# Performance work log

Measured on AMD Instinct MI355X. Metric: run time of the kernel, lower is better.

## Reference

```python
import jax, jax.numpy as jnp
import numpy as np

IN, H, OUT = 88, 200, 88


def lstm_layer(x, w_ih, w_hh, b_ih, b_hh):
    # x: [T, B, in]; weights in torch layout: w_ih [4H, in], w_hh [4H, H]
    # gate order (torch): i, f, g, o
    gx = jnp.einsum('tbi,gi->tbg', x, w_ih) + (b_ih + b_hh)  # precompute input gates
    B = x.shape[1]
    h0 = jnp.zeros((B, w_hh.shape[1]), x.dtype)
    c0 = jnp.zeros((B, w_hh.shape[1]), x.dtype)

    def step(carry, gxt):
        h, c = carry
        gates = gxt + h @ w_hh.T
        i, f, g, o = jnp.split(gates, 4, axis=-1)
        i = jax.nn.sigmoid(i)
        f = jax.nn.sigmoid(f)
        g = jnp.tanh(g)
        o = jax.nn.sigmoid(o)
        c = f * c + i * g
        h = o * jnp.tanh(c)
        return (h, c), h

    (hT, cT), ys = jax.lax.scan(step, (h0, c0), gx)
    return ys, hT, cT


def setup_inputs() -> dict:
    key = jax.random.key(0)
    ks = jax.random.split(key, 11)
    s = 1.0 / np.sqrt(H)
    u = lambda k, shape: jax.random.uniform(k, shape, jnp.float32, -s, s)
    T, B = 2048, 128
    x = (jax.random.uniform(ks[0], (T, B, IN)) > 0.9).astype(jnp.float32)  # sparse piano roll
    return {
        'x': x,
        'w_ih0': u(ks[1], (4 * H, IN)), 'w_hh0': u(ks[2], (4 * H, H)),
        'b_ih0': u(ks[3], (4 * H,)), 'b_hh0': u(ks[4], (4 * H,)),
        'w_ih1': u(ks[5], (4 * H, H)), 'w_hh1': u(ks[6], (4 * H, H)),
        'b_ih1': u(ks[7], (4 * H,)), 'b_hh1': u(ks[8], (4 * H,)),
        'w_fc': u(ks[9], (OUT, H)), 'b_fc': u(ks[10], (OUT,)),
    }


def reference(x, w_ih0, w_hh0, b_ih0, b_hh0, w_ih1, w_hh1, b_ih1, b_hh1, w_fc, b_fc):
    y0, h0n, c0n = lstm_layer(x, w_ih0, w_hh0, b_ih0, b_hh0)
    y1, h1n, c1n = lstm_layer(y0, w_ih1, w_hh1, b_ih1, b_hh1)
    out = jax.nn.sigmoid(jnp.einsum('tbh,oh->tbo', y1, w_fc) + b_fc)
    hn = jnp.stack([h0n, h1n])  # [2, B, H]
    cn = jnp.stack([c0n, c1n])
    return out, hn, cn
```

## Files before the change

### kernel.cpp

```cpp
#include <hip/hip_runtime.h>
#include <cstdint>
#include <cstddef>


#define TS    2048
#define BB    128
#define IN_D  88
#define HID   200
#define OUT_D 88
#define KX    96
#define KH    224
#define RING  4
#define FR    16
#define FSTR  32

typedef __attribute__((ext_vector_type(8))) short short8;
typedef __attribute__((ext_vector_type(4))) float f32x4;

constexpr int NW0 = 13, NW1 = 13;
constexpr int NWORK = NW0 + NW1 + 1;

__device__ inline unsigned short f2bf(float f){
  union{float f; unsigned u;} v; v.f = f;
  unsigned r = v.u + 0x7FFFu + ((v.u >> 16) & 1u);
  return (unsigned short)(r >> 16);
}
__device__ inline float sigf(float x){ return 1.0f/(1.0f + __expf(-x)); }
__device__ inline float tanhf2(float x){ return 2.0f/(1.0f + __expf(-2.0f*x)) - 1.0f; }

__device__ inline unsigned ld_flag(const unsigned* p){
  return __hip_atomic_load(p, __ATOMIC_RELAXED, __HIP_MEMORY_SCOPE_AGENT);
}
__device__ inline void post1(unsigned* p){
  __hip_atomic_fetch_add(p, 1u, __ATOMIC_RELAXED, __HIP_MEMORY_SCOPE_AGENT);
}
__device__ inline unsigned* fsl(unsigned* base, int t){ return base + (size_t)(t & (FR-1))*FSTR; }
__device__ inline unsigned ftg(int t, int nw){ return (unsigned)((t/FR + 1)*nw); }

__device__ inline void wg_wait2(int tid, unsigned* p0, unsigned v0,
                                unsigned* p1, unsigned v1){
  if (tid < 64 && (p0 || p1)){
    int n = 0;
    for(;;){
      unsigned a0 = p0 ? ld_flag(p0) : 0xFFFFFFFFu;
      unsigned a1 = p1 ? ld_flag(p1) : 0xFFFFFFFFu;
      bool ok = true;
      if (p0 && a0 < v0) ok = false;
      if (p1 && a1 < v1) ok = false;
      if (ok || ++n > 4000) break;
      __builtin_amdgcn_s_sleep(1);
    }
  }
  __syncthreads();
}

__device__ inline short8 loadB(const unsigned short* buf, int b, int kt, int q){
  const unsigned long long* p =
      (const unsigned long long*)(buf + ((size_t)kt*BB + b)*32 + q*8);
  unsigned long long lo = __hip_atomic_load(p,   __ATOMIC_RELAXED, __HIP_MEMORY_SCOPE_AGENT);
  unsigned long long hi = __hip_atomic_load(p+1, __ATOMIC_RELAXED, __HIP_MEMORY_SCOPE_AGENT);
  union{ unsigned long long u[2]; short8 s; } v; v.u[0]=lo; v.u[1]=hi;
  return v.s;
}

__device__ inline void cvt_x(const float4* pa, const float4* pb, int q, short8* xf){
  #pragma unroll
  for (int kt = 0; kt < 3; ++kt){
    int k = kt*32 + q*8;
    short8 r = {0,0,0,0,0,0,0,0};
    if (k + 8 <= IN_D){
      r[0]=(short)f2bf(pa[kt].x); r[1]=(short)f2bf(pa[kt].y);
      r[2]=(short)f2bf(pa[kt].z); r[3]=(short)f2bf(pa[kt].w);
      r[4]=(short)f2bf(pb[kt].x); r[5]=(short)f2bf(pb[kt].y);
      r[6]=(short)f2bf(pb[kt].z); r[7]=(short)f2bf(pb[kt].w);
    }
    xf[kt] = r;
  }
}

template<int ROLE>
__device__ void run_role(int j0,
    const float* __restrict__ xin,
    const float* __restrict__ wi, const float* __restrict__ wh,
    const float* __restrict__ bi, const float* __restrict__ bh,
    float* __restrict__ out,
    unsigned short* h0buf, unsigned short* h1buf,
    unsigned* f0p, unsigned* f0c, unsigned* f1p, unsigned* f1c,
    unsigned* f1g, unsigned* fFg,
    short* w_s, float* bias_s, unsigned short* hT)
{
  constexpr int ROWS = (ROLE==2)?96:64;
  constexpr int MT   = (ROLE==2)?6:4;
  constexpr int KTOT = (ROLE==0)?10:(ROLE==1?14:7);
  const int tid = threadIdx.x;

  constexpr int TOTW = KTOT*4*MT*16*8;
  for (int idx = tid; idx < TOTW; idx += 512){
    int e    = idx & 7;
    int nn_s = (idx >> 3) & 15;
    int rest = idx >> 7;
    int mt   = rest % MT;
    int qk   = rest / MT;
    int q_s  = qk & 3;
    int ktf  = qk >> 2;
    int r = mt*16 + nn_s;
    int k = ktf*32 + q_s*8 + e;
    float v = 0.f;
    if (ROLE == 2){
      if (r < OUT_D && k < HID) v = wi[r*HID + k];
    } else {
      int j = j0 + (r >> 2), g = r & 3;
      if (j < HID){
        int gr = g*HID + j;
        if (ROLE == 0){
          if (k < IN_D)                   v = wi[gr*IN_D + k];
          else if (k >= KX && k < KX+HID) v = wh[gr*HID + (k-KX)];
        } else {
          if (k < HID)                    v = wi[gr*HID + k];
          else if (k >= KH && k < KH+HID) v = wh[gr*HID + (k-KH)];
        }
      }
    }
    w_s[idx] = (short)f2bf(v);
  }
  for (int r = tid; r < ROWS; r += 512){
    float bv = 0.f;
    if (ROLE == 2){ if (r < OUT_D) bv = bi[r]; }
    else { int j = j0 + (r>>2), g = r&3; if (j < HID){ int gr = g*HID+j; bv = bi[gr] + bh[gr]; } }
    bias_s[r] = bv;
  }
  __syncthreads();

  const int lane = tid & 63;
  const int wv   = tid >> 6;
  const int q    = lane >> 4;
  const int nn   = lane & 15;
  const int b    = wv*16 + nn;

  const int wbase = (q*MT*16 + nn)*8;
  #define WS_FRAG(ktf, mt) (*(const short8*)&w_s[wbase + ((ktf)*4*MT + (mt))*128])

  float c[MT], hl[MT];
  #pragma unroll
  for (int i=0;i<MT;i++){ c[i]=0.f; hl[i]=0.f; }

  short8 xf[3];
  float4 pa[3], pb[3];
  if (ROLE == 0){
    #pragma unroll
    for (int kt=0;kt<3;kt++){
      int k = kt*32 + q*8;
      if (k + 8 <= IN_D){
        const float* xp = xin + (size_t)b*IN_D + k;
        pa[kt] = *(const float4*)xp; pb[kt] = *(const float4*)(xp + 4);
      }
    }
    cvt_x(pa, pb, q, xf);
  }

  for (int t = 0; t < TS; ++t){
    f32x4 acc[MT];
    #pragma unroll
    for (int mt=0; mt<MT; ++mt){
      #pragma unroll
      for (int r=0;r<4;r++) acc[mt][r] = bias_s[mt*16 + q*4 + r];
    }

    if (ROLE == 0){
      #pragma unroll
      for (int kt=0; kt<3; ++kt){
        #pragma unroll
        for (int mt=0; mt<MT; ++mt){
          acc[mt] = __builtin_amdgcn_mfma_f32_16x16x32_bf16(WS_FRAG(kt,mt), xf[kt], acc[mt], 0, 0, 0);
        }
      }
      if (t + 1 < TS){
        #pragma unroll
        for (int kt=0;kt<3;kt++){
          int k = kt*32 + q*8;
          if (k + 8 <= IN_D){
            const float* xp = xin + ((size_t)(t+1)*BB + b)*IN_D + k;
            pa[kt] = *(const float4*)xp; pb[kt] = *(const float4*)(xp + 4);
          }
        }
      }
      unsigned *p0=nullptr,*p1=nullptr; unsigned v0=0,v1=0;
      if (t >= 1){   p0 = fsl(f0p, t-1);    v0 = ftg(t-1, NW0); }
      if (t >= RING){p1 = fsl(f1g, t-RING); v1 = ftg(t-RING, NW1); }
      wg_wait2(tid, p0, v0, p1, v1);
      const unsigned short* hs = h0buf + (size_t)((t-1)&(RING-1))*(BB*KH);
      short8 bfr[7];
      #pragma unroll
      for (int kt=0;kt<7;kt++) bfr[kt] = loadB(hs, b, kt, q);
      #pragma unroll
      for (int kt=0;kt<7;kt++){
        #pragma unroll
        for (int mt=0; mt<MT; ++mt){
          acc[mt] = __builtin_amdgcn_mfma_f32_16x16x32_bf16(WS_FRAG(3+kt,mt), bfr[kt], acc[mt], 0, 0, 0);
        }
      }
    } else if (ROLE == 1){
      {
        unsigned *p1=nullptr; unsigned v1=0;
        if (t >= RING){ p1 = fsl(fFg, t-RING); v1 = ftg(t-RING, 1); }
        wg_wait2(tid, fsl(f0c, t), ftg(t, NW0), p1, v1);
      }
      const unsigned short* hs0 = h0buf + (size_t)(t&(RING-1))*(BB*KH);
      short8 bfr0[7];
      #pragma unroll
      for (int kt=0;kt<7;kt++) bfr0[kt] = loadB(hs0, b, kt, q);
      {
        unsigned *p0=nullptr; unsigned v0=0;
        if (t >= 1){ p0 = fsl(f1p, t-1); v0 = ftg(t-1, NW1); }
        wg_wait2(tid, p0, v0, nullptr, 0);
      }
      const unsigned short* hs1 = h1buf + (size_t)((t-1)&(RING-1))*(BB*KH);
      short8 bfr1[7];
      #pragma unroll
      for (int kt=0;kt<7;kt++) bfr1[kt] = loadB(hs1, b, kt, q);
      #pragma unroll
      for (int kt=0;kt<7;kt++){
        #pragma unroll
        for (int mt=0; mt<MT; ++mt){
          acc[mt] = __builtin_amdgcn_mfma_f32_16x16x32_bf16(WS_FRAG(kt,mt), bfr0[kt], acc[mt], 0, 0, 0);
        }
      }
      __syncthreads();
      if (tid == 0) post1(fsl(f1g, t));
      #pragma unroll
      for (int kt=0;kt<7;kt++){
        #pragma unroll
        for (int mt=0; mt<MT; ++mt){
          acc[mt] = __builtin_amdgcn_mfma_f32_16x16x32_bf16(WS_FRAG(7+kt,mt), bfr1[kt], acc[mt], 0, 0, 0);
        }
      }
    } else {
      wg_wait2(tid, fsl(f1c, t), ftg(t, NW1), nullptr, 0);
      const unsigned short* hs1 = h1buf + (size_t)(t&(RING-1))*(BB*KH);
      short8 bfr[7];
      #pragma unroll
      for (int kt=0;kt<7;kt++) bfr[kt] = loadB(hs1, b, kt, q);
      #pragma unroll
      for (int kt=0;kt<7;kt++){
        #pragma unroll
        for (int mt=0; mt<MT; ++mt){
          acc[mt] = __builtin_amdgcn_mfma_f32_16x16x32_bf16(WS_FRAG(kt,mt), bfr[kt], acc[mt], 0, 0, 0);
        }
      }
      __syncthreads();
      if (tid == 0) post1(fsl(fFg, t));
      #pragma unroll
      for (int mt=0; mt<MT; ++mt){
        #pragma unroll
        for (int r=0;r<4;r++){
          int o = mt*16 + q*4 + r;
          if (o < OUT_D) out[((size_t)t*BB + b)*OUT_D + o] = sigf(acc[mt][r]);
        }
      }
      continue;
    }

    #pragma unroll
    for (int mt=0; mt<MT; ++mt){
      float ii = sigf(acc[mt][0]);
      float ff = sigf(acc[mt][1]);
      float gg = tanhf2(acc[mt][2]);
      float oo = sigf(acc[mt][3]);
      c[mt] = ff*c[mt] + ii*gg;
      float h = oo * tanhf2(c[mt]);
      hl[mt] = h;
      hT[b*16 + mt*4 + q] = f2bf(h);
    }
    __syncthreads();
    {
      int bb = tid >> 2, ch = tid & 3;
      if (j0 + ch*4 < HID){
        unsigned long long v = *(const unsigned long long*)&hT[bb*16 + ch*4];
        int kt = j0 >> 5, off = j0 & 31;
        unsigned short* dst = (ROLE==0 ? h0buf : h1buf)
                            + (size_t)(t&(RING-1))*(BB*KH)
                            + ((size_t)kt*BB + bb)*32 + off + ch*4;
        __hip_atomic_store((unsigned long long*)dst, v,
                           __ATOMIC_RELAXED, __HIP_MEMORY_SCOPE_AGENT);
      }
    }
    asm volatile("s_waitcnt vmcnt(0)" ::: "memory");
    __syncthreads();
    if (tid == 0){
      if (ROLE == 0){ post1(fsl(f0p, t)); post1(fsl(f0c, t)); }
      else          { post1(fsl(f1p, t)); post1(fsl(f1c, t)); }
    }
    if (ROLE == 0) cvt_x(pa, pb, q, xf);
  }

  if (ROLE < 2){
    size_t base = (size_t)TS*BB*OUT_D;
    float* hn = out + base + (size_t)ROLE*(BB*HID);
    float* cn = out + base + 2*(size_t)BB*HID + (size_t)ROLE*(BB*HID);
    #pragma unroll
    for (int mt=0; mt<MT; ++mt){
      int unit = j0 + mt*4 + q;
      if (unit < HID){
        hn[b*HID + unit] = hl[mt];
        cn[b*HID + unit] = c[mt];
      }
    }
  }
  #undef WS_FRAG
}

__global__ __launch_bounds__(512, 2) void lstm_net(
    const float* __restrict__ x,
    const float* __restrict__ wih0, const float* __restrict__ whh0,
    const float* __restrict__ bih0, const float* __restrict__ bhh0,
    const float* __restrict__ wih1, const float* __restrict__ whh1,
    const float* __restrict__ bih1, const float* __restrict__ bhh1,
    const float* __restrict__ wfc,  const float* __restrict__ bfc,
    float* __restrict__ out,
    unsigned short* h0buf, unsigned short* h1buf,
    unsigned* f0p, unsigned* f0c, unsigned* f1p, unsigned* f1c,
    unsigned* f1g, unsigned* fFg)
{
  __shared__ short w_s[64*456];
  __shared__ float bias_s[96];
  __shared__ unsigned short hT[128*16];
  int wg = blockIdx.x;
  if (wg < NW0){
    run_role<0>(wg*16, x, wih0, whh0, bih0, bhh0, out, h0buf, h1buf,
                f0p, f0c, f1p, f1c, f1g, fFg, w_s, bias_s, hT);
  } else if (wg < NW0+NW1){
    run_role<1>((wg-NW0)*16, x, wih1, whh1, bih1, bhh1, out, h0buf, h1buf,
                f0p, f0c, f1p, f1c, f1g, fFg, w_s, bias_s, hT);
  } else {
    run_role<2>(0, x, wfc, nullptr, bfc, nullptr, out, h0buf, h1buf,
                f0p, f0c, f1p, f1c, f1g, fFg, w_s, bias_s, hT);
  }
}

extern "C" void kernel_launch(void* const* d_in, const int* in_sizes, int n_in,
                              void* d_out, int out_size, void* d_ws, size_t ws_size,
                              hipStream_t stream) {
  const float* x    = (const float*)d_in[0];
  const float* wih0 = (const float*)d_in[1];
  const float* whh0 = (const float*)d_in[2];
  const float* bih0 = (const float*)d_in[3];
  const float* bhh0 = (const float*)d_in[4];
  const float* wih1 = (const float*)d_in[5];
  const float* whh1 = (const float*)d_in[6];
  const float* bih1 = (const float*)d_in[7];
  const float* bhh1 = (const float*)d_in[8];
  const float* wfc  = (const float*)d_in[9];
  const float* bfc  = (const float*)d_in[10];
  float* out = (float*)d_out;

  char* ws = (char*)d_ws;
  const size_t HSZ = (size_t)RING * BB * KH * 2;
  const size_t FSZ = (size_t)FR * FSTR * 4;
  unsigned short* h0 = (unsigned short*)(ws + 0);
  unsigned short* h1 = (unsigned short*)(ws + HSZ);
  unsigned* f0p = (unsigned*)(ws + 2*HSZ + 0*FSZ);
  unsigned* f0c = (unsigned*)(ws + 2*HSZ + 1*FSZ);
  unsigned* f1p = (unsigned*)(ws + 2*HSZ + 2*FSZ);
  unsigned* f1c = (unsigned*)(ws + 2*HSZ + 3*FSZ);
  unsigned* f1g = (unsigned*)(ws + 2*HSZ + 4*FSZ);
  unsigned* fFg = (unsigned*)(ws + 2*HSZ + 5*FSZ);

  hipMemsetAsync(d_ws, 0, 2*HSZ + 6*FSZ, stream);
  hipLaunchKernelGGL(lstm_net, dim3(NWORK), dim3(512), 0, stream,
      x, wih0, whh0, bih0, bhh0, wih1, whh1, bih1, bhh1, wfc, bfc,
      out, h0, h1, f0p, f0c, f1p, f1c, f1g, fFg);
}
```

Measured before the change: 12.33 ms.

## Split layer-1 input projection into dedicated producer workgroups feeding recurrent workgroups

Adds 13 new workgroups that compute the layer-1 input-gate projection (W_ih1·h0 + bias) per timestep and write fp32 partial gates into a ring buffer with per-slice flags. The layer-1 recurrent workgroups now load only W_hh1 (halving their K depth), read the precomputed gates, and run just the h1 recurrent MFMAs. This takes the input projection off the layer-1 critical path so layer 1 no longer serialises on both matmuls each step. In exchange it adds extra global traffic, more flags and workgroups, and a longer spin timeout.

```diff
diff --git a/kernel.cpp b/kernel.cpp
--- a/kernel.cpp
+++ b/kernel.cpp
@@ -17,8 +17,8 @@
 typedef __attribute__((ext_vector_type(8))) short short8;
 typedef __attribute__((ext_vector_type(4))) float f32x4;
 
-constexpr int NW0 = 13, NW1 = 13;
-constexpr int NWORK = NW0 + NW1 + 1;
+constexpr int NW0 = 13, NWP = 13, NW1 = 13;
+constexpr int NWORK = NW0 + NWP + NW1 + 1;
 
 __device__ inline unsigned short f2bf(float f){
   union{float f; unsigned u;} v; v.f = f;
@@ -31,11 +31,21 @@
 __device__ inline unsigned ld_flag(const unsigned* p){
   return __hip_atomic_load(p, __ATOMIC_RELAXED, __HIP_MEMORY_SCOPE_AGENT);
 }
+__device__ inline void st_flag(unsigned* p, unsigned v){
+  __hip_atomic_store(p, v, __ATOMIC_RELAXED, __HIP_MEMORY_SCOPE_AGENT);
+}
 __device__ inline void post1(unsigned* p){
   __hip_atomic_fetch_add(p, 1u, __ATOMIC_RELAXED, __HIP_MEMORY_SCOPE_AGENT);
 }
 __device__ inline unsigned* fsl(unsigned* base, int t){ return base + (size_t)(t & (FR-1))*FSTR; }
 __device__ inline unsigned ftg(int t, int nw){ return (unsigned)((t/FR + 1)*nw); }
+
+__device__ inline unsigned long long ld64(const unsigned long long* p){
+  return __hip_atomic_load(p, __ATOMIC_RELAXED, __HIP_MEMORY_SCOPE_AGENT);
+}
+__device__ inline void st64(unsigned long long* p, unsigned long long v){
+  __hip_atomic_store(p, v, __ATOMIC_RELAXED, __HIP_MEMORY_SCOPE_AGENT);
+}
 
 __device__ inline void wg_wait2(int tid, unsigned* p0, unsigned v0,
                                 unsigned* p1, unsigned v1){
@@ -47,7 +57,7 @@
       bool ok = true;
       if (p0 && a0 < v0) ok = false;
       if (p1 && a1 < v1) ok = false;
-      if (ok || ++n > 4000) break;
+      if (ok || ++n > 20000) break;
       __builtin_amdgcn_s_sleep(1);
     }
   }
@@ -57,8 +67,8 @@
 __device__ inline short8 loadB(const unsigned short* buf, int b, int kt, int q){
   const unsigned long long* p =
       (const unsigned long long*)(buf + ((size_t)kt*BB + b)*32 + q*8);
-  unsigned long long lo = __hip_atomic_load(p,   __ATOMIC_RELAXED, __HIP_MEMORY_SCOPE_AGENT);
-  unsigned long long hi = __hip_atomic_load(p+1, __ATOMIC_RELAXED, __HIP_MEMORY_SCOPE_AGENT);
+  unsigned long long lo = ld64(p);
+  unsigned long long hi = ld64(p+1);
   union{ unsigned long long u[2]; short8 s; } v; v.u[0]=lo; v.u[1]=hi;
   return v.s;
 }
@@ -79,19 +89,19 @@
 }
 
 template<int ROLE>
-__device__ void run_role(int j0,
+__device__ void run_role(int j0, int pj,
     const float* __restrict__ xin,
     const float* __restrict__ wi, const float* __restrict__ wh,
     const float* __restrict__ bi, const float* __restrict__ bh,
     float* __restrict__ out,
-    unsigned short* h0buf, unsigned short* h1buf,
+    unsigned short* h0buf, unsigned short* h1buf, float* gxbuf,
     unsigned* f0p, unsigned* f0c, unsigned* f1p, unsigned* f1c,
-    unsigned* f1g, unsigned* fFg,
+    unsigned* f1g, unsigned* fFg, unsigned* fGp, unsigned* fGg,
     short* w_s, float* bias_s, unsigned short* hT)
 {
   constexpr int ROWS = (ROLE==2)?96:64;
   constexpr int MT   = (ROLE==2)?6:4;
-  constexpr int KTOT = (ROLE==0)?10:(ROLE==1?14:7);
+  constexpr int KTOT = (ROLE==0)?10:7;
   const int tid = threadIdx.x;
 
   constexpr int TOTW = KTOT*4*MT*16*8;
@@ -108,17 +118,18 @@
     float v = 0.f;
     if (ROLE == 2){
       if (r < OUT_D && k < HID) v = wi[r*HID + k];
-    } else {
+    } else if (ROLE == 0){
       int j = j0 + (r >> 2), g = r & 3;
       if (j < HID){
         int gr = g*HID + j;
-        if (ROLE == 0){
-          if (k < IN_D)                   v = wi[gr*IN_D + k];
-          else if (k >= KX && k < KX+HID) v = wh[gr*HID + (k-KX)];
-        } else {
-          if (k < HID)                    v = wi[gr*HID + k];
-          else if (k >= KH && k < KH+HID) v = wh[gr*HID + (k-KH)];
-        }
+        if (k < IN_D)                   v = wi[gr*IN_D + k];
+        else if (k >= KX && k < KX+HID) v = wh[gr*HID + (k-KX)];
+      }
+    } else {
+      int j = j0 + (r >> 2), g = r & 3;
+      if (j < HID && k < HID){
+        int gr = g*HID + j;
+        v = wi[gr*HID + k];
       }
     }
     w_s[idx] = (short)f2bf(v);
@@ -126,7 +137,10 @@
   for (int r = tid; r < ROWS; r += 512){
     float bv = 0.f;
     if (ROLE == 2){ if (r < OUT_D) bv = bi[r]; }
-    else { int j = j0 + (r>>2), g = r&3; if (j < HID){ int gr = g*HID+j; bv = bi[gr] + bh[gr]; } }
+    else if (ROLE != 1){
+      int j = j0 + (r>>2), g = r&3;
+      if (j < HID){ int gr = g*HID+j; bv = bi[gr] + bh[gr]; }
+    }
     bias_s[r] = bv;
   }
   __syncthreads();
@@ -159,11 +173,48 @@
   }
 
   for (int t = 0; t < TS; ++t){
+    if (ROLE == 3){
+      f32x4 acc[4];
+      #pragma unroll
+      for (int mt=0; mt<4; ++mt){
+        #pragma unroll
+        for (int r=0;r<4;r++) acc[mt][r] = bias_s[mt*16 + q*4 + r];
+      }
+      {
+        unsigned *p1=nullptr; unsigned v1=0;
+        if (t >= RING){ p1 = fsl(fGg, t-RING)+pj; v1 = (unsigned)(t-RING+1); }
+        wg_wait2(tid, fsl(f0c, t), ftg(t, NW0), p1, v1);
+      }
+      const unsigned short* hs0 = h0buf + (size_t)(t&(RING-1))*(BB*KH);
+      short8 bfr0[7];
+      #pragma unroll
+      for (int kt=0;kt<7;kt++) bfr0[kt] = loadB(hs0, b, kt, q);
+      #pragma unroll
+      for (int kt=0;kt<7;kt++){
+        #pragma unroll
+        for (int mt=0; mt<4; ++mt){
+          acc[mt] = __builtin_amdgcn_mfma_f32_16x16x32_bf16(WS_FRAG(kt,mt), bfr0[kt], acc[mt], 0, 0, 0);
+        }
+      }
+      float* gd = gxbuf + (((size_t)(t&(RING-1))*NWP + pj)*512 + tid)*16;
+      union{ f32x4 v[4]; unsigned long long u[8]; } g;
+      #pragma unroll
+      for (int mt=0;mt<4;mt++) g.v[mt]=acc[mt];
+      #pragma unroll
+      for (int i=0;i<8;i++) st64(((unsigned long long*)gd)+i, g.u[i]);
+      asm volatile("s_waitcnt vmcnt(0)" ::: "memory");
+      __syncthreads();
+      if (tid == 0){ st_flag(fsl(fGp,t)+pj, (unsigned)(t+1)); post1(fsl(f1g,t)); }
+      continue;
+    }
+
     f32x4 acc[MT];
-    #pragma unroll
-    for (int mt=0; mt<MT; ++mt){
-      #pragma unroll
-      for (int r=0;r<4;r++) acc[mt][r] = bias_s[mt*16 + q*4 + r];
+    if (ROLE != 1){
+      #pragma unroll
+      for (int mt=0; mt<MT; ++mt){
+        #pragma unroll
+        for (int r=0;r<4;r++) acc[mt][r] = bias_s[mt*16 + q*4 + r];
+      }
     }
 
     if (ROLE == 0){
@@ -186,7 +237,7 @@
       }
       unsigned *p0=nullptr,*p1=nullptr; unsigned v0=0,v1=0;
       if (t >= 1){   p0 = fsl(f0p, t-1);    v0 = ftg(t-1, NW0); }
-      if (t >= RING){p1 = fsl(f1g, t-RING); v1 = ftg(t-RING, NW1); }
+      if (t >= RING){p1 = fsl(f1g, t-RING); v1 = ftg(t-RING, NWP); }
       wg_wait2(tid, p0, v0, p1, v1);
       const unsigned short* hs = h0buf + (size_t)((t-1)&(RING-1))*(BB*KH);
       short8 bfr[7];
@@ -203,35 +254,24 @@
       {
         unsigned *p1=nullptr; unsigned v1=0;
         if (t >= RING){ p1 = fsl(fFg, t-RING); v1 = ftg(t-RING, 1); }
-        wg_wait2(tid, fsl(f0c, t), ftg(t, NW0), p1, v1);
-      }
-      const unsigned short* hs0 = h0buf + (size_t)(t&(RING-1))*(BB*KH);
-      short8 bfr0[7];
-      #pragma unroll
-      for (int kt=0;kt<7;kt++) bfr0[kt] = loadB(hs0, b, kt, q);
-      {
-        unsigned *p0=nullptr; unsigned v0=0;
-        if (t >= 1){ p0 = fsl(f1p, t-1); v0 = ftg(t-1, NW1); }
-        wg_wait2(tid, p0, v0, nullptr, 0);
-      }
+        wg_wait2(tid, fsl(fGp,t)+pj, (unsigned)(t+1), p1, v1);
+      }
+      if (t >= 1) wg_wait2(tid, fsl(f1p, t-1), ftg(t-1, NW1), nullptr, 0);
+      const float* gs = gxbuf + (((size_t)(t&(RING-1))*NWP + pj)*512 + tid)*16;
+      union{ f32x4 v[4]; unsigned long long u[8]; } g;
+      #pragma unroll
+      for (int i=0;i<8;i++) g.u[i] = ld64(((const unsigned long long*)gs)+i);
       const unsigned short* hs1 = h1buf + (size_t)((t-1)&(RING-1))*(BB*KH);
       short8 bfr1[7];
       #pragma unroll
       for (int kt=0;kt<7;kt++) bfr1[kt] = loadB(hs1, b, kt, q);
       #pragma unroll
+      for (int mt=0;mt<MT;mt++) acc[mt] = g.v[mt];
+      #pragma unroll
       for (int kt=0;kt<7;kt++){
         #pragma unroll
         for (int mt=0; mt<MT; ++mt){
-          acc[mt] = __builtin_amdgcn_mfma_f32_16x16x32_bf16(WS_FRAG(kt,mt), bfr0[kt], acc[mt], 0, 0, 0);
-        }
-      }
-      __syncthreads();
-      if (tid == 0) post1(fsl(f1g, t));
-      #pragma unroll
-      for (int kt=0;kt<7;kt++){
-        #pragma unroll
-        for (int mt=0; mt<MT; ++mt){
-          acc[mt] = __builtin_amdgcn_mfma_f32_16x16x32_bf16(WS_FRAG(7+kt,mt), bfr1[kt], acc[mt], 0, 0, 0);
+          acc[mt] = __builtin_amdgcn_mfma_f32_16x16x32_bf16(WS_FRAG(kt,mt), bfr1[kt], acc[mt], 0, 0, 0);
         }
       }
     } else {
@@ -280,23 +320,24 @@
         unsigned short* dst = (ROLE==0 ? h0buf : h1buf)
                             + (size_t)(t&(RING-1))*(BB*KH)
                             + ((size_t)kt*BB + bb)*32 + off + ch*4;
-        __hip_atomic_store((unsigned long long*)dst, v,
-                           __ATOMIC_RELAXED, __HIP_MEMORY_SCOPE_AGENT);
+        st64((unsigned long long*)dst, v);
       }
     }
     asm volatile("s_waitcnt vmcnt(0)" ::: "memory");
     __syncthreads();
     if (tid == 0){
       if (ROLE == 0){ post1(fsl(f0p, t)); post1(fsl(f0c, t)); }
-      else          { post1(fsl(f1p, t)); post1(fsl(f1c, t)); }
+      else          { post1(fsl(f1p, t)); post1(fsl(f1c, t));
+                      st_flag(fsl(fGg,t)+pj, (unsigned)(t+1)); }
     }
     if (ROLE == 0) cvt_x(pa, pb, q, xf);
   }
 
-  if (ROLE < 2){
+  if (ROLE == 0 || ROLE == 1){
     size_t base = (size_t)TS*BB*OUT_D;
-    float* hn = out + base + (size_t)ROLE*(BB*HID);
-    float* cn = out + base + 2*(size_t)BB*HID + (size_t)ROLE*(BB*HID);
+    constexpr int L = (ROLE==0)?0:1;
+    float* hn = out + base + (size_t)L*(BB*HID);
+    float* cn = out + base + 2*(size_t)BB*HID + (size_t)L*(BB*HID);
     #pragma unroll
     for (int mt=0; mt<MT; ++mt){
       int unit = j0 + mt*4 + q;
@@ -317,23 +358,28 @@
     const float* __restrict__ bih1, const float* __restrict__ bhh1,
     const float* __restrict__ wfc,  const float* __restrict__ bfc,
     float* __restrict__ out,
-    unsigned short* h0buf, unsigned short* h1buf,
+    unsigned short* h0buf, unsigned short* h1buf, float* gxbuf,
     unsigned* f0p, unsigned* f0c, unsigned* f1p, unsigned* f1c,
-    unsigned* f1g, unsigned* fFg)
+    unsigned* f1g, unsigned* fFg, unsigned* fGp, unsigned* fGg)
 {
   __shared__ short w_s[64*456];
   __shared__ float bias_s[96];
   __shared__ unsigned short hT[128*16];
   int wg = blockIdx.x;
   if (wg < NW0){
-    run_role<0>(wg*16, x, wih0, whh0, bih0, bhh0, out, h0buf, h1buf,
-                f0p, f0c, f1p, f1c, f1g, fFg, w_s, bias_s, hT);
-  } else if (wg < NW0+NW1){
-    run_role<1>((wg-NW0)*16, x, wih1, whh1, bih1, bhh1, out, h0buf, h1buf,
-                f0p, f0c, f1p, f1c, f1g, fFg, w_s, bias_s, hT);
+    run_role<0>(wg*16, 0, x, wih0, whh0, bih0, bhh0, out, h0buf, h1buf, gxbuf,
+                f0p, f0c, f1p, f1c, f1g, fFg, fGp, fGg, w_s, bias_s, hT);
+  } else if (wg < NW0+NWP){
+    int j = wg - NW0;
+    run_role<3>(j*16, j, x, wih1, nullptr, bih1, bhh1, out, h0buf, h1buf, gxbuf,
+                f0p, f0c, f1p, f1c, f1g, fFg, fGp, fGg, w_s, bias_s, hT);
+  } else if (wg < NW0+NWP+NW1){
+    int j = wg - NW0 - NWP;
+    run_role<1>(j*16, j, x, whh1, nullptr, nullptr, nullptr, out, h0buf, h1buf, gxbuf,
+                f0p, f0c, f1p, f1c, f1g, fFg, fGp, fGg, w_s, bias_s, hT);
   } else {
-    run_role<2>(0, x, wfc, nullptr, bfc, nullptr, out, h0buf, h1buf,
-                f0p, f0c, f1p, f1c, f1g, fFg, w_s, bias_s, hT);
+    run_role<2>(0, 0, x, wfc, nullptr, bfc, nullptr, out, h0buf, h1buf, gxbuf,
+                f0p, f0c, f1p, f1c, f1g, fFg, fGp, fGg, w_s, bias_s, hT);
   }
 }
 
@@ -354,8 +400,9 @@
   float* out = (float*)d_out;
 
   char* ws = (char*)d_ws;
-  const size_t HSZ = (size_t)RING * BB * KH * 2;
-  const size_t FSZ = (size_t)FR * FSTR * 4;
+  const size_t HSZ  = (size_t)RING * BB * KH * 2;
+  const size_t FSZ  = (size_t)FR * FSTR * 4;
+  const size_t GXSZ = (size_t)RING * NWP * 512 * 16 * 4;
   unsigned short* h0 = (unsigned short*)(ws + 0);
   unsigned short* h1 = (unsigned short*)(ws + HSZ);
   unsigned* f0p = (unsigned*)(ws + 2*HSZ + 0*FSZ);
@@ -364,9 +411,13 @@
   unsigned* f1c = (unsigned*)(ws + 2*HSZ + 3*FSZ);
   unsigned* f1g = (unsigned*)(ws + 2*HSZ + 4*FSZ);
   unsigned* fFg = (unsigned*)(ws + 2*HSZ + 5*FSZ);
-
-  hipMemsetAsync(d_ws, 0, 2*HSZ + 6*FSZ, stream);
+  unsigned* fGp = (unsigned*)(ws + 2*HSZ + 6*FSZ);
+  unsigned* fGg = (unsigned*)(ws + 2*HSZ + 7*FSZ);
+  float* gx = (float*)(ws + 2*HSZ + 8*FSZ);
+
+  hipMemsetAsync(d_ws, 0, 2*HSZ + 8*FSZ, stream);
+  (void)GXSZ;
   hipLaunchKernelGGL(lstm_net, dim3(NWORK), dim3(512), 0, stream,
       x, wih0, whh0, bih0, bhh0, wih1, whh1, bih1, bhh1, wfc, bfc,
-      out, h0, h1, f0p, f0c, f1p, f1c, f1g, fFg);
-}
+      out, h0, h1, gx, f0p, f0c, f1p, f1c, f1g, fFg, fGp, fGg);
+}
```

Result: faster. 11.98 ms (-2.9%).
